# Kernel optimization log

Measured on AMD Instinct MI355X. Metric: run time of the kernel, lower is better.

## Reference

```python
import jax, jax.numpy as jnp
import numpy as np

N_NODES = 65536
IN_DIM = 512
OUT_DIM = 512
N_EDGES = 524288
BN_EPS = 1e-5
NORM_EPS = 1e-6


def setup_inputs() -> dict:
    key = jax.random.key(0)
    k1, k2, k3, k4 = jax.random.split(key, 4)
    features = jax.random.normal(k1, (N_NODES, IN_DIM), dtype=jnp.float32)
    edge_index = jax.random.randint(k2, (2, N_EDGES), 0, N_NODES, dtype=jnp.int64)
    # torch Linear weight layout: [out_features, in_features] with in = 2*IN_DIM
    W = jax.random.normal(k3, (OUT_DIM, 2 * IN_DIM), dtype=jnp.float32) * (1.0 / np.sqrt(2 * IN_DIM))
    b = jax.random.normal(k4, (OUT_DIM,), dtype=jnp.float32) * 0.01
    gamma = jnp.ones((OUT_DIM,), dtype=jnp.float32)
    beta = jnp.zeros((OUT_DIM,), dtype=jnp.float32)
    running_mean = jnp.zeros((OUT_DIM,), dtype=jnp.float32)
    running_var = jnp.ones((OUT_DIM,), dtype=jnp.float32)
    return {
        "features": features,
        "edge_index": edge_index,
        "W": W,
        "b": b,
        "gamma": gamma,
        "beta": beta,
        "running_mean": running_mean,
        "running_var": running_var,
    }


def reference(features, edge_index, W, b, gamma, beta, running_mean, running_var):
    sources = edge_index[0]
    targets = edge_index[1]
    # scatter-sum of neighbor (target) features into source rows  [N, D]
    aggregated = jax.ops.segment_sum(features[targets], sources, num_segments=N_NODES)
    out = jnp.concatenate([features, aggregated], axis=1)  # [N, 2D]
    out = out @ W.T + b  # [N, OUT_DIM]
    out = jax.nn.relu(out)
    # BatchNorm1d (eval mode, running stats)
    out = (out - running_mean) * jax.lax.rsqrt(running_var + BN_EPS) * gamma + beta
    # dropout is identity in inference
    out = out / (jnp.linalg.norm(out, axis=1, keepdims=True) + NORM_EPS)
    return out
```

## Files before the change

### kernel.cpp

```cpp
#include <hip/hip_runtime.h>
#include <hip/hip_bf16.h>

#define N_NODES 65536
#define DIM 512
#define N_EDGES 524288
#define BN_EPS 1e-5f
#define NORM_EPS 1e-6f

typedef __attribute__((ext_vector_type(8))) short short8;
typedef __attribute__((ext_vector_type(4))) float f32x4;

static __device__ __forceinline__ unsigned f2bf(float f) {
    union { float f; unsigned u; } c; c.f = f;
    unsigned u = c.u;
    return (u + 0x7fffu + ((u >> 16) & 1u)) >> 16;
}
static __device__ __forceinline__ float bf16lo(unsigned u) {
    union { unsigned u; float f; } c; c.u = u << 16; return c.f;
}
static __device__ __forceinline__ float bf16hi(unsigned u) {
    union { unsigned u; float f; } c; c.u = u & 0xffff0000u; return c.f;
}
static __device__ __forceinline__ uint4 pack8(float4 a, float4 b) {
    uint4 o;
    o.x = f2bf(a.x) | (f2bf(a.y) << 16);
    o.y = f2bf(a.z) | (f2bf(a.w) << 16);
    o.z = f2bf(b.x) | (f2bf(b.y) << 16);
    o.w = f2bf(b.z) | (f2bf(b.w) << 16);
    return o;
}

__global__ void convert_kernel(const float* __restrict__ src,
                               unsigned short* __restrict__ dst, int n8) {
    int i = blockIdx.x * blockDim.x + threadIdx.x;
    if (i < n8) {
        const float4* s = (const float4*)src + i * 2;
        float4 f0 = s[0], f1 = s[1];
        ((uint4*)dst)[i] = pack8(f0, f1);
    }
}

__global__ void hist_kernel(const int* __restrict__ src, int* __restrict__ counts) {
    int e = blockIdx.x * blockDim.x + threadIdx.x;
    if (e < N_EDGES) atomicAdd(&counts[src[e]], 1);
}

__global__ void scan_partial(const int* __restrict__ counts, int* __restrict__ partials) {
    __shared__ int ws[4];
    int t = threadIdx.x;
    int v = counts[blockIdx.x * 256 + t];
#pragma unroll
    for (int d = 1; d < 64; d <<= 1) v += __shfl_xor(v, d);
    if ((t & 63) == 0) ws[t >> 6] = v;
    __syncthreads();
    if (t == 0) partials[blockIdx.x] = ws[0] + ws[1] + ws[2] + ws[3];
}

__global__ void scan_base(int* __restrict__ partials) {
    __shared__ int lds[256];
    int t = threadIdx.x;
    int v = partials[t];
    lds[t] = v;
    __syncthreads();
    for (int d = 1; d < 256; d <<= 1) {
        int mine = lds[t];
        int add = (t >= d) ? lds[t - d] : 0;
        __syncthreads();
        lds[t] = mine + add;
        __syncthreads();
    }
    partials[t] = lds[t] - v;
}

__global__ void scan_final(const int* __restrict__ counts,
                           const int* __restrict__ partials,
                           int* __restrict__ offsets, int* __restrict__ cursor) {
    __shared__ int lds[256];
    int t = threadIdx.x, b = blockIdx.x;
    int v = counts[b * 256 + t];
    lds[t] = v;
    __syncthreads();
    for (int d = 1; d < 256; d <<= 1) {
        int mine = lds[t];
        int add = (t >= d) ? lds[t - d] : 0;
        __syncthreads();
        lds[t] = mine + add;
        __syncthreads();
    }
    int excl = lds[t] - v + partials[b];
    offsets[b * 256 + t] = excl;
    cursor[b * 256 + t] = excl;
    if (b == 255 && t == 255) offsets[N_NODES] = excl + v;
}

__global__ void scatter_kernel(const int* __restrict__ src, const int* __restrict__ tgt,
                               int* __restrict__ cursor, int* __restrict__ sortedT) {
    int e = blockIdx.x * blockDim.x + threadIdx.x;
    if (e < N_EDGES) {
        int s = src[e];
        int pos = atomicAdd(&cursor[s], 1);
        sortedT[pos] = tgt[e];
    }
}

__global__ void aggregate_kernel(const unsigned short* __restrict__ Xb,
                                 const int* __restrict__ offsets,
                                 const int* __restrict__ sortedT,
                                 unsigned short* __restrict__ agg) {
    int wave = (blockIdx.x * blockDim.x + threadIdx.x) >> 6;
    int lane = threadIdx.x & 63;
    if (wave >= N_NODES) return;
    int beg = offsets[wave], end = offsets[wave + 1];
    float a[8] = {0.f, 0.f, 0.f, 0.f, 0.f, 0.f, 0.f, 0.f};
    const uint4* F = (const uint4*)Xb;
    for (int i = beg; i < end; ++i) {
        int t = sortedT[i];
        uint4 v = F[t * 64 + lane];
        a[0] += bf16lo(v.x); a[1] += bf16hi(v.x);
        a[2] += bf16lo(v.y); a[3] += bf16hi(v.y);
        a[4] += bf16lo(v.z); a[5] += bf16hi(v.z);
        a[6] += bf16lo(v.w); a[7] += bf16hi(v.w);
    }
    uint4 o;
    o.x = f2bf(a[0]) | (f2bf(a[1]) << 16);
    o.y = f2bf(a[2]) | (f2bf(a[3]) << 16);
    o.z = f2bf(a[4]) | (f2bf(a[5]) << 16);
    o.w = f2bf(a[6]) | (f2bf(a[7]) << 16);
    ((uint4*)agg)[wave * 64 + lane] = o;
}

__global__ __launch_bounds__(512, 4) void fused_gemm_norm_kernel(
        const unsigned short* __restrict__ Xb,
        const unsigned short* __restrict__ agg,
        const unsigned short* __restrict__ Wb,
        const float* __restrict__ bias,
        const float* __restrict__ gamma,
        const float* __restrict__ beta,
        const float* __restrict__ rmean,
        const float* __restrict__ rvar,
        float* __restrict__ out) {
    __shared__ uint4 Alds[512];
    __shared__ uint4 Blds[4096];
    __shared__ float ssm[64][8];

    const int t = threadIdx.x;
    const int m0 = blockIdx.x * 64;
    const int w = t >> 6, L = t & 63;
    const int ml = L & 15, quad = L >> 4;
    const int wn = w * 64;

    f32x4 acc[4][4];
#pragma unroll
    for (int mi = 0; mi < 4; ++mi)
#pragma unroll
        for (int ni = 0; ni < 4; ++ni)
            acc[mi][ni] = (f32x4){0.f, 0.f, 0.f, 0.f};

    for (int kt = 0; kt < 16; ++kt) {
        const unsigned short* Asrc = (kt < 8) ? (Xb + kt * 64) : (agg + (kt - 8) * 64);
        __syncthreads();
        {
            int c = t;
            int r = c >> 3, pp = c & 7;
            int p = pp ^ (r & 7);
            const unsigned short* ga = Asrc + (m0 + r) * 512 + p * 8;
            char* la = (char*)Alds + (t & 448) * 16;
            __builtin_amdgcn_global_load_lds(
                (const __attribute__((address_space(1))) unsigned int*)ga,
                (__attribute__((address_space(3))) unsigned int*)la, 16, 0, 0);
        }
#pragma unroll
        for (int j = 0; j < 8; ++j) {
            int c = j * 512 + t;
            int r = c >> 3, pp = c & 7;
            int p = pp ^ (r & 7);
            const unsigned short* gb = Wb + r * 1024 + kt * 64 + p * 8;
            char* lb = (char*)Blds + (j * 512 + (t & 448)) * 16;
            __builtin_amdgcn_global_load_lds(
                (const __attribute__((address_space(1))) unsigned int*)gb,
                (__attribute__((address_space(3))) unsigned int*)lb, 16, 0, 0);
        }
        __syncthreads();
#pragma unroll
        for (int kc = 0; kc < 2; ++kc) {
            int g = kc * 4 + quad;
            short8 a[4], b[4];
#pragma unroll
            for (int mi = 0; mi < 4; ++mi) {
                int ra = mi * 16 + ml;
                a[mi] = *(const short8*)&Alds[ra * 8 + (g ^ (ra & 7))];
                int rb = wn + mi * 16 + ml;
                b[mi] = *(const short8*)&Blds[rb * 8 + (g ^ (rb & 7))];
            }
#pragma unroll
            for (int mi = 0; mi < 4; ++mi)
#pragma unroll
                for (int ni = 0; ni < 4; ++ni)
                    acc[mi][ni] = __builtin_amdgcn_mfma_f32_16x16x32_bf16(
                        a[mi], b[ni], acc[mi][ni], 0, 0, 0);
        }
    }

    float bi[4], sc[4], sh[4];
#pragma unroll
    for (int ni = 0; ni < 4; ++ni) {
        int col = wn + ni * 16 + ml;
        bi[ni] = bias[col];
        sc[ni] = gamma[col] * __frsqrt_rn(rvar[col] + BN_EPS);
        sh[ni] = beta[col] - rmean[col] * sc[ni];
    }
    float ss[4][4];
#pragma unroll
    for (int mi = 0; mi < 4; ++mi)
#pragma unroll
        for (int r = 0; r < 4; ++r)
            ss[mi][r] = 0.f;
#pragma unroll
    for (int mi = 0; mi < 4; ++mi)
#pragma unroll
        for (int ni = 0; ni < 4; ++ni)
#pragma unroll
            for (int r = 0; r < 4; ++r) {
                float v = fmaxf(acc[mi][ni][r] + bi[ni], 0.f) * sc[ni] + sh[ni];
                acc[mi][ni][r] = v;
                ss[mi][r] += v * v;
            }
#pragma unroll
    for (int mi = 0; mi < 4; ++mi)
#pragma unroll
        for (int r = 0; r < 4; ++r) {
#pragma unroll
            for (int d = 1; d < 16; d <<= 1)
                ss[mi][r] += __shfl_xor(ss[mi][r], d);
        }
    if (ml == 0) {
#pragma unroll
        for (int mi = 0; mi < 4; ++mi)
#pragma unroll
            for (int r = 0; r < 4; ++r)
                ssm[mi * 16 + quad * 4 + r][w] = ss[mi][r];
    }
    __syncthreads();
#pragma unroll
    for (int mi = 0; mi < 4; ++mi)
#pragma unroll
        for (int r = 0; r < 4; ++r) {
            int rl = mi * 16 + quad * 4 + r;
            const float4* sp = (const float4*)ssm[rl];
            float4 s0 = sp[0], s1 = sp[1];
            float tot = s0.x + s0.y + s0.z + s0.w + s1.x + s1.y + s1.z + s1.w;
            float inv = 1.f / (sqrtf(tot) + NORM_EPS);
            int m = m0 + rl;
#pragma unroll
            for (int ni = 0; ni < 4; ++ni)
                out[m * 512 + wn + ni * 16 + ml] = acc[mi][ni][r] * inv;
        }
}

extern "C" void kernel_launch(void* const* d_in, const int* in_sizes, int n_in,
                              void* d_out, int out_size, void* d_ws, size_t ws_size,
                              hipStream_t stream) {
    const float* features = (const float*)d_in[0];
    const int* edges      = (const int*)d_in[1];
    const float* W        = (const float*)d_in[2];
    const float* bias     = (const float*)d_in[3];
    const float* gamma    = (const float*)d_in[4];
    const float* beta     = (const float*)d_in[5];
    const float* rmean    = (const float*)d_in[6];
    const float* rvar     = (const float*)d_in[7];
    float* out = (float*)d_out;

    char* ws = (char*)d_ws;
    int* counts   = (int*)(ws);
    int* offsets  = (int*)(ws + 0x100000);
    int* cursor   = (int*)(ws + 0x200000);
    int* partials = (int*)(ws + 0x280000);
    int* sortedT  = (int*)(ws + 0x300000);
    unsigned short* Wb  = (unsigned short*)(ws + 0x500000);
    unsigned short* Xb  = (unsigned short*)(ws + 0x600000);
    unsigned short* agg = (unsigned short*)(ws + 0x4600000);

    const int* src = edges;
    const int* tgt = edges + N_EDGES;

    hipMemsetAsync(counts, 0, N_NODES * sizeof(int), stream);
    hist_kernel<<<N_EDGES / 256, 256, 0, stream>>>(src, counts);
    scan_partial<<<256, 256, 0, stream>>>(counts, partials);
    scan_base<<<1, 256, 0, stream>>>(partials);
    scan_final<<<256, 256, 0, stream>>>(counts, partials, offsets, cursor);
    scatter_kernel<<<N_EDGES / 256, 256, 0, stream>>>(src, tgt, cursor, sortedT);
    convert_kernel<<<(N_NODES * DIM / 8) / 256, 256, 0, stream>>>(features, Xb, N_NODES * DIM / 8);
    convert_kernel<<<(DIM * 2 * DIM / 8) / 256, 256, 0, stream>>>(W, Wb, DIM * 2 * DIM / 8);
    aggregate_kernel<<<N_NODES / 4, 256, 0, stream>>>(Xb, offsets, sortedT, agg);
    fused_gemm_norm_kernel<<<N_NODES / 64, 512, 0, stream>>>(
        Xb, agg, Wb, bias, gamma, beta, rmean, rvar, out);
}
```

Before: 451.4 us.

## Fuse prep kernels, merge scan stages, unroll aggregation gathers, hoist BN params

Merges the feature/weight bf16 conversions and the edge histogram into one launch, and folds the single-block partial scan into each final-scan block by having every block redo the 256-entry scan. The aggregation loop is unrolled by four with two accumulator sets so more independent gathers are in flight at once. Bias and BatchNorm parameter loads in the GEMM are moved before the main loop. Together these cut launch count and gather latency, at the cost of redundant scan work in every block and extra registers in the GEMM.

```diff
diff --git a/kernel.cpp b/kernel.cpp
--- a/kernel.cpp
+++ b/kernel.cpp
@@ -30,19 +30,29 @@
     return o;
 }
 
-__global__ void convert_kernel(const float* __restrict__ src,
-                               unsigned short* __restrict__ dst, int n8) {
-    int i = blockIdx.x * blockDim.x + threadIdx.x;
-    if (i < n8) {
-        const float4* s = (const float4*)src + i * 2;
-        float4 f0 = s[0], f1 = s[1];
-        ((uint4*)dst)[i] = pack8(f0, f1);
-    }
-}
-
-__global__ void hist_kernel(const int* __restrict__ src, int* __restrict__ counts) {
-    int e = blockIdx.x * blockDim.x + threadIdx.x;
-    if (e < N_EDGES) atomicAdd(&counts[src[e]], 1);
+#define NB_CONVF 16384
+#define NB_CONVW 256
+#define NB_HIST  2048
+
+__global__ void prep_kernel(const float* __restrict__ features,
+                            unsigned short* __restrict__ Xb,
+                            const float* __restrict__ W,
+                            unsigned short* __restrict__ Wb,
+                            const int* __restrict__ src,
+                            int* __restrict__ counts) {
+    int b = blockIdx.x;
+    if (b < NB_CONVF) {
+        int i = b * 256 + threadIdx.x;
+        const float4* s = (const float4*)features + i * 2;
+        ((uint4*)Xb)[i] = pack8(s[0], s[1]);
+    } else if (b < NB_CONVF + NB_CONVW) {
+        int i = (b - NB_CONVF) * 256 + threadIdx.x;
+        const float4* s = (const float4*)W + i * 2;
+        ((uint4*)Wb)[i] = pack8(s[0], s[1]);
+    } else {
+        int e = (b - NB_CONVF - NB_CONVW) * 256 + threadIdx.x;
+        atomicAdd(&counts[src[e]], 1);
+    }
 }
 
 __global__ void scan_partial(const int* __restrict__ counts, int* __restrict__ partials) {
@@ -56,38 +66,28 @@
     if (t == 0) partials[blockIdx.x] = ws[0] + ws[1] + ws[2] + ws[3];
 }
 
-__global__ void scan_base(int* __restrict__ partials) {
+__global__ void scan_final2(const int* __restrict__ counts,
+                            const int* __restrict__ partials,
+                            int* __restrict__ offsets, int* __restrict__ cursor) {
     __shared__ int lds[256];
-    int t = threadIdx.x;
-    int v = partials[t];
+    __shared__ int pl[256];
+    int t = threadIdx.x, b = blockIdx.x;
+    int v = counts[b * 256 + t];
     lds[t] = v;
+    pl[t] = partials[t];
     __syncthreads();
     for (int d = 1; d < 256; d <<= 1) {
         int mine = lds[t];
         int add = (t >= d) ? lds[t - d] : 0;
+        int pm = pl[t];
+        int pa = (t >= d) ? pl[t - d] : 0;
         __syncthreads();
         lds[t] = mine + add;
+        pl[t] = pm + pa;
         __syncthreads();
     }
-    partials[t] = lds[t] - v;
-}
-
-__global__ void scan_final(const int* __restrict__ counts,
-                           const int* __restrict__ partials,
-                           int* __restrict__ offsets, int* __restrict__ cursor) {
-    __shared__ int lds[256];
-    int t = threadIdx.x, b = blockIdx.x;
-    int v = counts[b * 256 + t];
-    lds[t] = v;
-    __syncthreads();
-    for (int d = 1; d < 256; d <<= 1) {
-        int mine = lds[t];
-        int add = (t >= d) ? lds[t - d] : 0;
-        __syncthreads();
-        lds[t] = mine + add;
-        __syncthreads();
-    }
-    int excl = lds[t] - v + partials[b];
+    int base = (b > 0) ? pl[b - 1] : 0;
+    int excl = lds[t] - v + base;
     offsets[b * 256 + t] = excl;
     cursor[b * 256 + t] = excl;
     if (b == 255 && t == 255) offsets[N_NODES] = excl + v;
@@ -101,6 +101,13 @@
         int pos = atomicAdd(&cursor[s], 1);
         sortedT[pos] = tgt[e];
     }
+}
+
+static __device__ __forceinline__ void acc8(float* a, uint4 v) {
+    a[0] += bf16lo(v.x); a[1] += bf16hi(v.x);
+    a[2] += bf16lo(v.y); a[3] += bf16hi(v.y);
+    a[4] += bf16lo(v.z); a[5] += bf16hi(v.z);
+    a[6] += bf16lo(v.w); a[7] += bf16hi(v.w);
 }
 
 __global__ void aggregate_kernel(const unsigned short* __restrict__ Xb,
@@ -112,15 +119,31 @@
     if (wave >= N_NODES) return;
     int beg = offsets[wave], end = offsets[wave + 1];
     float a[8] = {0.f, 0.f, 0.f, 0.f, 0.f, 0.f, 0.f, 0.f};
+    float b[8] = {0.f, 0.f, 0.f, 0.f, 0.f, 0.f, 0.f, 0.f};
     const uint4* F = (const uint4*)Xb;
-    for (int i = beg; i < end; ++i) {
-        int t = sortedT[i];
-        uint4 v = F[t * 64 + lane];
-        a[0] += bf16lo(v.x); a[1] += bf16hi(v.x);
-        a[2] += bf16lo(v.y); a[3] += bf16hi(v.y);
-        a[4] += bf16lo(v.z); a[5] += bf16hi(v.z);
-        a[6] += bf16lo(v.w); a[7] += bf16hi(v.w);
-    }
+    int i = beg;
+    for (; i + 4 <= end; i += 4) {
+        int t0 = sortedT[i], t1 = sortedT[i + 1], t2 = sortedT[i + 2], t3 = sortedT[i + 3];
+        uint4 v0 = F[t0 * 64 + lane];
+        uint4 v1 = F[t1 * 64 + lane];
+        uint4 v2 = F[t2 * 64 + lane];
+        uint4 v3 = F[t3 * 64 + lane];
+        acc8(a, v0); acc8(b, v1); acc8(a, v2); acc8(b, v3);
+    }
+    if (i + 2 <= end) {
+        int t0 = sortedT[i], t1 = sortedT[i + 1];
+        uint4 v0 = F[t0 * 64 + lane];
+        uint4 v1 = F[t1 * 64 + lane];
+        acc8(a, v0); acc8(b, v1);
+        i += 2;
+    }
+    if (i < end) {
+        int t0 = sortedT[i];
+        uint4 v0 = F[t0 * 64 + lane];
+        acc8(a, v0);
+    }
+#pragma unroll
+    for (int k = 0; k < 8; ++k) a[k] += b[k];
     uint4 o;
     o.x = f2bf(a[0]) | (f2bf(a[1]) << 16);
     o.y = f2bf(a[2]) | (f2bf(a[3]) << 16);
@@ -149,6 +172,15 @@
     const int ml = L & 15, quad = L >> 4;
     const int wn = w * 64;
 
+    float bi[4], sc[4], sh[4];
+#pragma unroll
+    for (int ni = 0; ni < 4; ++ni) {
+        int col = wn + ni * 16 + ml;
+        bi[ni] = bias[col];
+        sc[ni] = gamma[col] * __frsqrt_rn(rvar[col] + BN_EPS);
+        sh[ni] = beta[col] - rmean[col] * sc[ni];
+    }
+
     f32x4 acc[4][4];
 #pragma unroll
     for (int mi = 0; mi < 4; ++mi)
@@ -160,8 +192,7 @@
         const unsigned short* Asrc = (kt < 8) ? (Xb + kt * 64) : (agg + (kt - 8) * 64);
         __syncthreads();
         {
-            int c = t;
-            int r = c >> 3, pp = c & 7;
+            int r = t >> 3, pp = t & 7;
             int p = pp ^ (r & 7);
             const unsigned short* ga = Asrc + (m0 + r) * 512 + p * 8;
             char* la = (char*)Alds + (t & 448) * 16;
@@ -201,14 +232,6 @@
         }
     }
 
-    float bi[4], sc[4], sh[4];
-#pragma unroll
-    for (int ni = 0; ni < 4; ++ni) {
-        int col = wn + ni * 16 + ml;
-        bi[ni] = bias[col];
-        sc[ni] = gamma[col] * __frsqrt_rn(rvar[col] + BN_EPS);
-        sh[ni] = beta[col] - rmean[col] * sc[ni];
-    }
     float ss[4][4];
 #pragma unroll
     for (int mi = 0; mi < 4; ++mi)
@@ -284,13 +307,11 @@
     const int* tgt = edges + N_EDGES;
 
     hipMemsetAsync(counts, 0, N_NODES * sizeof(int), stream);
-    hist_kernel<<<N_EDGES / 256, 256, 0, stream>>>(src, counts);
+    prep_kernel<<<NB_CONVF + NB_CONVW + NB_HIST, 256, 0, stream>>>(
+        features, Xb, W, Wb, src, counts);
     scan_partial<<<256, 256, 0, stream>>>(counts, partials);
-    scan_base<<<1, 256, 0, stream>>>(partials);
-    scan_final<<<256, 256, 0, stream>>>(counts, partials, offsets, cursor);
+    scan_final2<<<256, 256, 0, stream>>>(counts, partials, offsets, cursor);
     scatter_kernel<<<N_EDGES / 256, 256, 0, stream>>>(src, tgt, cursor, sortedT);
-    convert_kernel<<<(N_NODES * DIM / 8) / 256, 256, 0, stream>>>(features, Xb, N_NODES * DIM / 8);
-    convert_kernel<<<(DIM * 2 * DIM / 8) / 256, 256, 0, stream>>>(W, Wb, DIM * 2 * DIM / 8);
     aggregate_kernel<<<N_NODES / 4, 256, 0, stream>>>(Xb, offsets, sortedT, agg);
     fused_gemm_norm_kernel<<<N_NODES / 64, 512, 0, stream>>>(
         Xb, agg, Wb, bias, gamma, beta, rmean, rvar, out);
```

After: 441.0 us. 2.3% less time.
